# Kernel tuning notes

Hardware: AMD Instinct MI355X
Metric: run time of the kernel (lower is better)

The kernel has to match this reference:

```python
import jax, jax.numpy as jnp
import numpy as np

BATCH = 4096
LATENT = 2048
ZDIM = 128
TEMP = 0.5
PRIOR = 0.3
PRIOR_PRIME = 0.5
GAMMA = 1.0
BETA = 0.0
EPS = 1e-8  # torch CosineSimilarity eps


def setup_inputs() -> dict:
    key = jax.random.key(0)
    k = jax.random.split(key, 6)
    return {
        "h_i": jax.random.normal(k[0], (BATCH, LATENT), dtype=jnp.float32),
        "h_j": jax.random.normal(k[1], (BATCH, LATENT), dtype=jnp.float32),
        "z_i": jax.random.normal(k[2], (BATCH, ZDIM), dtype=jnp.float32),
        "z_j": jax.random.normal(k[3], (BATCH, ZDIM), dtype=jnp.float32),
        "target": jax.random.randint(k[4], (BATCH, 1), 0, 2, dtype=jnp.int64 if jax.config.jax_enable_x64 else jnp.int32),
        "W": jax.random.normal(k[5], (1, LATENT), dtype=jnp.float32) * (1.0 / np.sqrt(LATENT)),
        "b": jnp.zeros((1,), dtype=jnp.float32),
        "weight_onnpu": jnp.asarray(0.5, dtype=jnp.float32),
    }


def _onnpu_loss(inp, target):
    # inp: [B, 1] classifier logit; target: [B, 1] in {0, 1} -> {-1, +1}
    t = (target * 2 - 1).astype(inp.dtype)
    positive = (t == 1).astype(inp.dtype)
    unlabeled = (t == -1).astype(inp.dtype)
    one = jnp.asarray(1.0, inp.dtype)
    n_pos = jnp.maximum(one, jnp.sum(positive))
    n_unl = jnp.maximum(one, jnp.sum(unlabeled))
    sig = jax.nn.sigmoid  # loss(x) = sigmoid(-x)
    y_pos = sig(-(positive * inp)) * positive
    y_pos_inv = sig(positive * inp) * positive
    y_unl = sig(unlabeled * inp) * unlabeled
    positive_risk = PRIOR_PRIME / n_pos * jnp.sum(y_pos)
    negative_risk = ((1.0 - PRIOR_PRIME) / (n_unl * (1.0 - PRIOR)) * jnp.sum(y_unl)
                     - (1.0 - PRIOR_PRIME) * PRIOR / (n_pos * (1.0 - PRIOR)) * jnp.sum(y_pos_inv))
    # nnPU correction (nnPU=True, beta=0, gamma=1)
    return jnp.where(negative_risk < -BETA, -GAMMA * negative_risk,
                     positive_risk + negative_risk)


def _nt_xent_loss(z_i, z_j):
    B = z_i.shape[0]
    N = 2 * B
    z = jnp.concatenate([z_i, z_j], axis=0)  # [N, D]
    zn = z / jnp.maximum(jnp.linalg.norm(z, axis=1, keepdims=True), EPS)
    sim = (zn @ zn.T) / TEMP  # [N, N] cosine similarity / temperature
    idx = jnp.arange(N)
    pos = sim[idx, (idx + B) % N]  # positive pair logit per row
    # CE over [positive | all-other-than-self]: denominator is logsumexp over
    # the row with the self-similarity (diagonal) excluded.
    sim_masked = jnp.where(idx[:, None] == idx[None, :], -jnp.inf, sim)
    lse = jax.nn.logsumexp(sim_masked, axis=1)
    return jnp.sum(lse - pos) / N


def reference(h_i, h_j, z_i, z_j, target, W, b, weight_onnpu):
    logit_i = h_i @ W.T + b  # [B, 1]
    logit_j = h_j @ W.T + b
    onnpu_l = 0.5 * (_onnpu_loss(logit_i, target) + _onnpu_loss(logit_j, target))
    nt_xent_l = _nt_xent_loss(z_i, z_j)
    return weight_onnpu * onnpu_l + (1.0 - weight_onnpu) * nt_xent_l
```

## Files before the change

### kernel.cpp

```cpp
#include <hip/hip_runtime.h>

#define BATCH  4096
#define NROWS  8192
#define LATENT 2048
#define ZDIM   128
#define PRIORc       0.3f
#define PRIOR_PRIMEc 0.5f

#define NSIM 2080

typedef __attribute__((ext_vector_type(8))) short bf16x8;
typedef __attribute__((ext_vector_type(4))) float f32x4;

__device__ inline unsigned short f2bf_rne(float f) {
    unsigned int u = __float_as_uint(f);
    u = u + 0x7fffu + ((u >> 16) & 1u);
    return (unsigned short)(u >> 16);
}

__device__ inline float wave_reduce_sum(float v) {
#pragma unroll
    for (int m = 1; m < 64; m <<= 1) v += __shfl_xor(v, m, 64);
    return v;
}

__device__ inline void gload_lds16(const void* g, void* l) {
    __builtin_amdgcn_global_load_lds(
        (const __attribute__((address_space(1))) unsigned int*)g,
        (__attribute__((address_space(3))) unsigned int*)l, 16, 0, 0);
}

#define ZSCALE 1.69864464f

__global__ void k_zprep(const float* __restrict__ z_i, const float* __restrict__ z_j,
                        unsigned short* __restrict__ znb, float* __restrict__ pos,
                        float* __restrict__ dexp, float* __restrict__ S_row) {
    int bid = blockIdx.x;
    int wave = threadIdx.x >> 6, lane = threadIdx.x & 63;
    if (threadIdx.x < 8) S_row[bid * 8 + threadIdx.x] = 0.f;
    int r = bid * 4 + wave;
    int p = r + BATCH;
    float2 a = ((const float2*)(z_i + (size_t)r * ZDIM))[lane];
    float2 c = ((const float2*)(z_j + (size_t)r * ZDIM))[lane];
    float sa = wave_reduce_sum(a.x * a.x + a.y * a.y);
    float sc = wave_reduce_sum(c.x * c.x + c.y * c.y);
    float dd = wave_reduce_sum(a.x * c.x + a.y * c.y);
    float inva = 1.f / fmaxf(sqrtf(sa), 1e-8f);
    float invc = 1.f / fmaxf(sqrtf(sc), 1e-8f);
    if (lane == 0) {
        float pv = 2.0f * dd * inva * invc;
        pos[r] = pv;
        pos[p] = pv;
    }
    int kt = lane >> 4;
    int q  = (lane >> 2) & 3;
    int j  = (lane & 3) * 2;
    int lrow = q * 16;
    float fa = inva * ZSCALE, fc = invc * ZSCALE;
    ushort2 wa; wa.x = f2bf_rne(a.x * fa); wa.y = f2bf_rne(a.y * fa);
    ushort2 wc; wc.x = f2bf_rne(c.x * fc); wc.y = f2bf_rne(c.y * fc);
    {
        size_t off = ((size_t)((r >> 4) * 4 + kt) * 64 + (lrow + (r & 15))) * 8 + j;
        *(ushort2*)(znb + off) = wa;
    }
    {
        size_t off = ((size_t)((p >> 4) * 4 + kt) * 64 + (lrow + (p & 15))) * 8 + j;
        *(ushort2*)(znb + off) = wc;
    }
    float ax = __uint_as_float((unsigned)wa.x << 16);
    float ay = __uint_as_float((unsigned)wa.y << 16);
    float cx = __uint_as_float((unsigned)wc.x << 16);
    float cy = __uint_as_float((unsigned)wc.y << 16);
    float da = wave_reduce_sum(ax * ax + ay * ay);
    float dc = wave_reduce_sum(cx * cx + cy * cy);
    if (lane == 0) {
        dexp[r] = __builtin_amdgcn_exp2f(da);
        dexp[p] = __builtin_amdgcn_exp2f(dc);
    }
}

__global__ void __launch_bounds__(256, 4) k_main(
        const unsigned short* __restrict__ znb, float* __restrict__ S_row,
        const float* __restrict__ h_i, const float* __restrict__ h_j,
        const float* __restrict__ W, const float* __restrict__ bb,
        float* __restrict__ logits) {
    int bid = blockIdx.x;
    int lane = threadIdx.x & 63, wave = threadIdx.x >> 6;
    if (bid < NSIM) {
        int k = bid;
        int i = (int)((129.0f - sqrtf(16641.0f - 8.0f * (float)k)) * 0.5f);
        if (i > 63) i = 63;
        while (i * (129 - i) / 2 > k) --i;
        while ((i + 1) * (128 - i) / 2 <= k) ++i;
        int j = i + (k - i * (129 - i) / 2);
        bool diag = (i == j);

        int q = lane >> 4, t = lane & 15;
        int row0 = i * 128 + (wave >> 1) * 64;
        int gA = row0 >> 4;

        __shared__ __align__(16) unsigned char bpan[32768];
        __shared__ float red[256];

        {
            const unsigned char* gsrc = (const unsigned char*)znb + (size_t)j * 32768;
#pragma unroll
            for (int u = 0; u < 8; ++u) {
                int boff = u * 4096 + wave * 1024 + lane * 16;
                gload_lds16(gsrc + boff, bpan + u * 4096 + wave * 1024);
            }
        }
        red[threadIdx.x] = 0.f;

        const bf16x8* zf = (const bf16x8*)znb;
        bf16x8 a[4][4];
#pragma unroll
        for (int mt = 0; mt < 4; ++mt)
#pragma unroll
            for (int kt = 0; kt < 4; ++kt)
                a[mt][kt] = zf[(size_t)((gA + mt) * 4 + kt) * 64 + lane];

        float s[16];
#pragma unroll
        for (int idx = 0; idx < 16; ++idx) s[idx] = 0.f;
        float c[4];

        __syncthreads();

#pragma unroll
        for (int nt = 0; nt < 4; ++nt) {
            bf16x8 b[4];
#pragma unroll
            for (int kt = 0; kt < 4; ++kt)
                b[kt] = *(const bf16x8*)(bpan +
                        ((size_t)(((wave & 1) * 4 + nt) * 4 + kt) * 1024) + lane * 16);
            f32x4 acc[4];
            f32x4 zero = {0.f, 0.f, 0.f, 0.f};
#pragma unroll
            for (int mt = 0; mt < 4; ++mt) acc[mt] = zero;
#pragma unroll
            for (int kt = 0; kt < 4; ++kt)
#pragma unroll
                for (int mt = 0; mt < 4; ++mt)
                    acc[mt] = __builtin_amdgcn_mfma_f32_16x16x32_bf16(a[mt][kt], b[kt], acc[mt], 0, 0, 0);
            float csum = 0.f;
#pragma unroll
            for (int mt = 0; mt < 4; ++mt)
#pragma unroll
                for (int reg = 0; reg < 4; ++reg) {
                    float e = __builtin_amdgcn_exp2f(acc[mt][reg]);
                    s[mt * 4 + reg] += e;
                    csum += e;
                }
            c[nt] = csum;
        }

#pragma unroll
        for (int idx = 0; idx < 16; ++idx) {
            float v = s[idx];
            v += __shfl_xor(v, 1, 64);
            v += __shfl_xor(v, 2, 64);
            v += __shfl_xor(v, 4, 64);
            v += __shfl_xor(v, 8, 64);
            if (t == 0)
                atomicAdd(&red[(wave >> 1) * 64 + (idx >> 2) * 16 + q * 4 + (idx & 3)], v);
        }
#pragma unroll
        for (int nt = 0; nt < 4; ++nt) {
            float v = c[nt];
            v += __shfl_xor(v, 16, 64);
            v += __shfl_xor(v, 32, 64);
            if (q == 0)
                atomicAdd(&red[128 + (wave & 1) * 64 + nt * 16 + t], v);
        }
        __syncthreads();
        if (threadIdx.x < 128) {
            atomicAdd(&S_row[i * 128 + threadIdx.x], red[threadIdx.x]);
        } else if (!diag) {
            atomicAdd(&S_row[j * 128 + (threadIdx.x & 127)], red[threadIdx.x]);
        }
    } else {
        int r = (bid - NSIM) * 4 + wave;
        const float* h = (r < BATCH) ? (h_i + (size_t)r * LATENT)
                                     : (h_j + (size_t)(r - BATCH) * LATENT);
        const f32x4* h4 = (const f32x4*)h;
        const f32x4* w4 = (const f32x4*)W;
        float s = 0.f;
#pragma unroll
        for (int itr = 0; itr < 8; ++itr) {
            f32x4 av = h4[itr * 64 + lane];
            f32x4 wv = w4[itr * 64 + lane];
            s += av.x * wv.x + av.y * wv.y + av.z * wv.z + av.w * wv.w;
        }
        s = wave_reduce_sum(s);
        if (lane == 0) logits[r] = s + bb[0];
    }
}

__global__ void k_final(const float* __restrict__ S_row, const float* __restrict__ pos,
                        const float* __restrict__ dexp, const float* __restrict__ logits,
                        const int* __restrict__ target,
                        const float* __restrict__ w_onnpu, float* __restrict__ out) {
    float nt_s = 0.f;
    for (int r = threadIdx.x; r < NROWS; r += 1024)
        nt_s += __logf(S_row[r] - dexp[r]) - pos[r];
    float v[8];
#pragma unroll
    for (int i = 0; i < 8; ++i) v[i] = 0.f;
    for (int r = threadIdx.x; r < BATCH; r += 1024) {
        float li = logits[r], lj = logits[BATCH + r];
        bool p = (target[r] == 1);
        float si_n = 1.f / (1.f + __expf(li));
        float si_p = 1.f / (1.f + __expf(-li));
        float sj_n = 1.f / (1.f + __expf(lj));
        float sj_p = 1.f / (1.f + __expf(-lj));
        v[0] += p ? 1.f : 0.f;
        v[1] += p ? 0.f : 1.f;
        v[2] += p ? si_n : 0.f;
        v[3] += p ? si_p : 0.f;
        v[4] += p ? 0.f : si_p;
        v[5] += p ? sj_n : 0.f;
        v[6] += p ? sj_p : 0.f;
        v[7] += p ? 0.f : sj_p;
    }
    __shared__ float red[16][9];
    int wave = threadIdx.x >> 6, lane = threadIdx.x & 63;
    nt_s = wave_reduce_sum(nt_s);
#pragma unroll
    for (int i = 0; i < 8; ++i) v[i] = wave_reduce_sum(v[i]);
    if (lane == 0) {
        red[wave][0] = nt_s;
#pragma unroll
        for (int i = 0; i < 8; ++i) red[wave][1 + i] = v[i];
    }
    __syncthreads();
    if (threadIdx.x == 0) {
        float t[9];
#pragma unroll
        for (int i = 0; i < 9; ++i) {
            float acc = 0.f;
#pragma unroll
            for (int wv = 0; wv < 16; ++wv) acc += red[wv][i];
            t[i] = acc;
        }
        float ntxent = t[0] / (float)NROWS;
        float np = fmaxf(1.f, t[1]), nu = fmaxf(1.f, t[2]);
        float pr_i = PRIOR_PRIMEc / np * t[3];
        float nr_i = (1.f - PRIOR_PRIMEc) / (nu * (1.f - PRIORc)) * t[5]
                   - (1.f - PRIOR_PRIMEc) * PRIORc / (np * (1.f - PRIORc)) * t[4];
        float li_loss = (nr_i < 0.f) ? -nr_i : (pr_i + nr_i);
        float pr_j = PRIOR_PRIMEc / np * t[6];
        float nr_j = (1.f - PRIOR_PRIMEc) / (nu * (1.f - PRIORc)) * t[8]
                   - (1.f - PRIOR_PRIMEc) * PRIORc / (np * (1.f - PRIORc)) * t[7];
        float lj_loss = (nr_j < 0.f) ? -nr_j : (pr_j + nr_j);
        float onnpu = 0.5f * (li_loss + lj_loss);
        float w = w_onnpu[0];
        out[0] = w * onnpu + (1.f - w) * ntxent;
    }
}

extern "C" void kernel_launch(void* const* d_in, const int* in_sizes, int n_in,
                              void* d_out, int out_size, void* d_ws, size_t ws_size,
                              hipStream_t stream) {
    const float* h_i = (const float*)d_in[0];
    const float* h_j = (const float*)d_in[1];
    const float* z_i = (const float*)d_in[2];
    const float* z_j = (const float*)d_in[3];
    const int* target = (const int*)d_in[4];
    const float* W = (const float*)d_in[5];
    const float* b = (const float*)d_in[6];
    const float* w_onnpu = (const float*)d_in[7];

    char* ws = (char*)d_ws;
    unsigned short* znb = (unsigned short*)ws;
    float* S_row  = (float*)(ws + 2097152);
    float* pos    = (float*)(ws + 2097152 + 32768);
    float* logits = (float*)(ws + 2097152 + 65536);
    float* dexp   = (float*)(ws + 2097152 + 98304);
    float* out = (float*)d_out;

    k_zprep<<<1024, 256, 0, stream>>>(z_i, z_j, znb, pos, dexp, S_row);
    k_main<<<NSIM + 2048, 256, 0, stream>>>(znb, S_row, h_i, h_j, W, b, logits);
    k_final<<<1, 1024, 0, stream>>>(S_row, pos, dexp, logits, target, w_onnpu, out);
}
```

Baseline: 132.1 us.

## Make similarity blocks persistent over paired stripes with double-buffered LDS panels

The similarity part now runs as 512 persistent blocks instead of 2080 one-tile blocks. Each group of 16 blocks handles a complementary pair of row stripes (i and 63-i) to balance the triangular workload. Each block iterates over tiles while double-buffering the B panel in LDS via async global-to-LDS loads. Row sums stay in registers across tiles of the same stripe and are flushed with global atomics, replacing the per-block LDS reduction, while column sums go straight to global atomics. This amortizes launch and A-fragment loads and overlaps loads with compute, at the cost of doubled LDS (occupancy drops to 2 blocks per CU) and more global atomic traffic.

```diff
diff --git a/kernel.cpp b/kernel.cpp
--- a/kernel.cpp
+++ b/kernel.cpp
@@ -7,7 +7,8 @@
 #define PRIORc       0.3f
 #define PRIOR_PRIMEc 0.5f
 
-#define NSIM 2080
+#define NSIMB 512
+#define NGEMV 2048
 
 typedef __attribute__((ext_vector_type(8))) short bf16x8;
 typedef __attribute__((ext_vector_type(4))) float f32x4;
@@ -79,80 +80,129 @@
     }
 }
 
-__global__ void __launch_bounds__(256, 4) k_main(
+__global__ void __launch_bounds__(256, 2) k_main(
         const unsigned short* __restrict__ znb, float* __restrict__ S_row,
         const float* __restrict__ h_i, const float* __restrict__ h_j,
         const float* __restrict__ W, const float* __restrict__ bb,
         float* __restrict__ logits) {
     int bid = blockIdx.x;
     int lane = threadIdx.x & 63, wave = threadIdx.x >> 6;
-    if (bid < NSIM) {
-        int k = bid;
-        int i = (int)((129.0f - sqrtf(16641.0f - 8.0f * (float)k)) * 0.5f);
-        if (i > 63) i = 63;
-        while (i * (129 - i) / 2 > k) --i;
-        while ((i + 1) * (128 - i) / 2 <= k) ++i;
-        int j = i + (k - i * (129 - i) / 2);
-        bool diag = (i == j);
-
+    if (bid < NSIMB) {
+        int pairIdx = bid >> 4;
+        int sub = bid & 15;
+        int i0 = pairIdx, i1 = 63 - pairIdx;
+        int n0 = 64 - i0;
         int q = lane >> 4, t = lane & 15;
-        int row0 = i * 128 + (wave >> 1) * 64;
-        int gA = row0 >> 4;
-
-        __shared__ __align__(16) unsigned char bpan[32768];
-        __shared__ float red[256];
+        const bf16x8* zf = (const bf16x8*)znb;
+
+        __shared__ __align__(16) unsigned char bpan[2][32768];
 
         {
-            const unsigned char* gsrc = (const unsigned char*)znb + (size_t)j * 32768;
-#pragma unroll
-            for (int u = 0; u < 8; ++u) {
-                int boff = u * 4096 + wave * 1024 + lane * 16;
-                gload_lds16(gsrc + boff, bpan + u * 4096 + wave * 1024);
+            int j0 = i0 + sub;
+            const unsigned char* gsrc = (const unsigned char*)znb + (size_t)j0 * 32768;
+#pragma unroll
+            for (int u = 0; u < 8; ++u)
+                gload_lds16(gsrc + u * 4096 + wave * 1024 + lane * 16,
+                            bpan[0] + u * 4096 + wave * 1024);
+        }
+
+        int stripe = i0;
+        bf16x8 a[4][4];
+        {
+            int gA = i0 * 8 + (wave >> 1) * 4;
+#pragma unroll
+            for (int mt = 0; mt < 4; ++mt)
+#pragma unroll
+                for (int kt = 0; kt < 4; ++kt)
+                    a[mt][kt] = zf[(size_t)((gA + mt) * 4 + kt) * 64 + lane];
+        }
+
+        float s[16];
+#pragma unroll
+        for (int idx = 0; idx < 16; ++idx) s[idx] = 0.f;
+
+        __syncthreads();
+
+        int buf = 0;
+        for (int p = sub; p < 65; p += 16) {
+            int pi = (p < n0) ? i0 : i1;
+            int pj = (p < n0) ? (i0 + p) : (i1 + (p - n0));
+
+            int pn = p + 16;
+            if (pn < 65) {
+                int nj = (pn < n0) ? (i0 + pn) : (i1 + (pn - n0));
+                const unsigned char* gsrc = (const unsigned char*)znb + (size_t)nj * 32768;
+#pragma unroll
+                for (int u = 0; u < 8; ++u)
+                    gload_lds16(gsrc + u * 4096 + wave * 1024 + lane * 16,
+                                bpan[buf ^ 1] + u * 4096 + wave * 1024);
             }
-        }
-        red[threadIdx.x] = 0.f;
-
-        const bf16x8* zf = (const bf16x8*)znb;
-        bf16x8 a[4][4];
-#pragma unroll
-        for (int mt = 0; mt < 4; ++mt)
-#pragma unroll
-            for (int kt = 0; kt < 4; ++kt)
-                a[mt][kt] = zf[(size_t)((gA + mt) * 4 + kt) * 64 + lane];
-
-        float s[16];
-#pragma unroll
-        for (int idx = 0; idx < 16; ++idx) s[idx] = 0.f;
-        float c[4];
-
-        __syncthreads();
-
-#pragma unroll
-        for (int nt = 0; nt < 4; ++nt) {
-            bf16x8 b[4];
-#pragma unroll
-            for (int kt = 0; kt < 4; ++kt)
-                b[kt] = *(const bf16x8*)(bpan +
-                        ((size_t)(((wave & 1) * 4 + nt) * 4 + kt) * 1024) + lane * 16);
-            f32x4 acc[4];
-            f32x4 zero = {0.f, 0.f, 0.f, 0.f};
-#pragma unroll
-            for (int mt = 0; mt < 4; ++mt) acc[mt] = zero;
-#pragma unroll
-            for (int kt = 0; kt < 4; ++kt)
+
+            if (pi != stripe) {
+#pragma unroll
+                for (int idx = 0; idx < 16; ++idx) {
+                    float v = s[idx];
+                    v += __shfl_xor(v, 1, 64);
+                    v += __shfl_xor(v, 2, 64);
+                    v += __shfl_xor(v, 4, 64);
+                    v += __shfl_xor(v, 8, 64);
+                    if (t == 0)
+                        atomicAdd(&S_row[stripe * 128 + (wave >> 1) * 64 +
+                                         (idx >> 2) * 16 + q * 4 + (idx & 3)], v);
+                }
+                stripe = pi;
+                int gA = pi * 8 + (wave >> 1) * 4;
 #pragma unroll
                 for (int mt = 0; mt < 4; ++mt)
-                    acc[mt] = __builtin_amdgcn_mfma_f32_16x16x32_bf16(a[mt][kt], b[kt], acc[mt], 0, 0, 0);
-            float csum = 0.f;
-#pragma unroll
-            for (int mt = 0; mt < 4; ++mt)
-#pragma unroll
-                for (int reg = 0; reg < 4; ++reg) {
-                    float e = __builtin_amdgcn_exp2f(acc[mt][reg]);
-                    s[mt * 4 + reg] += e;
-                    csum += e;
+#pragma unroll
+                    for (int kt = 0; kt < 4; ++kt)
+                        a[mt][kt] = zf[(size_t)((gA + mt) * 4 + kt) * 64 + lane];
+#pragma unroll
+                for (int idx = 0; idx < 16; ++idx) s[idx] = 0.f;
+            }
+
+            float c[4];
+#pragma unroll
+            for (int nt = 0; nt < 4; ++nt) {
+                bf16x8 b[4];
+#pragma unroll
+                for (int kt = 0; kt < 4; ++kt)
+                    b[kt] = *(const bf16x8*)(bpan[buf] +
+                            ((size_t)(((wave & 1) * 4 + nt) * 4 + kt) * 1024) + lane * 16);
+                f32x4 acc[4];
+                f32x4 zero = {0.f, 0.f, 0.f, 0.f};
+#pragma unroll
+                for (int mt = 0; mt < 4; ++mt) acc[mt] = zero;
+#pragma unroll
+                for (int kt = 0; kt < 4; ++kt)
+#pragma unroll
+                    for (int mt = 0; mt < 4; ++mt)
+                        acc[mt] = __builtin_amdgcn_mfma_f32_16x16x32_bf16(a[mt][kt], b[kt], acc[mt], 0, 0, 0);
+                float csum = 0.f;
+#pragma unroll
+                for (int mt = 0; mt < 4; ++mt)
+#pragma unroll
+                    for (int reg = 0; reg < 4; ++reg) {
+                        float e = __builtin_amdgcn_exp2f(acc[mt][reg]);
+                        s[mt * 4 + reg] += e;
+                        csum += e;
+                    }
+                c[nt] = csum;
+            }
+
+            if (pi != pj) {
+#pragma unroll
+                for (int nt = 0; nt < 4; ++nt) {
+                    float v = c[nt];
+                    v += __shfl_xor(v, 16, 64);
+                    v += __shfl_xor(v, 32, 64);
+                    if (q == 0)
+                        atomicAdd(&S_row[pj * 128 + (wave & 1) * 64 + nt * 16 + t], v);
                 }
-            c[nt] = csum;
+            }
+
+            __syncthreads();
+            buf ^= 1;
         }
 
 #pragma unroll
@@ -163,24 +213,11 @@
             v += __shfl_xor(v, 4, 64);
             v += __shfl_xor(v, 8, 64);
             if (t == 0)
-                atomicAdd(&red[(wave >> 1) * 64 + (idx >> 2) * 16 + q * 4 + (idx & 3)], v);
-        }
-#pragma unroll
-        for (int nt = 0; nt < 4; ++nt) {
-            float v = c[nt];
-            v += __shfl_xor(v, 16, 64);
-            v += __shfl_xor(v, 32, 64);
-            if (q == 0)
-                atomicAdd(&red[128 + (wave & 1) * 64 + nt * 16 + t], v);
-        }
-        __syncthreads();
-        if (threadIdx.x < 128) {
-            atomicAdd(&S_row[i * 128 + threadIdx.x], red[threadIdx.x]);
-        } else if (!diag) {
-            atomicAdd(&S_row[j * 128 + (threadIdx.x & 127)], red[threadIdx.x]);
+                atomicAdd(&S_row[stripe * 128 + (wave >> 1) * 64 +
+                                 (idx >> 2) * 16 + q * 4 + (idx & 3)], v);
         }
     } else {
-        int r = (bid - NSIM) * 4 + wave;
+        int r = (bid - NSIMB) * 4 + wave;
         const float* h = (r < BATCH) ? (h_i + (size_t)r * LATENT)
                                      : (h_j + (size_t)(r - BATCH) * LATENT);
         const f32x4* h4 = (const f32x4*)h;
@@ -280,6 +317,6 @@
     float* out = (float*)d_out;
 
     k_zprep<<<1024, 256, 0, stream>>>(z_i, z_j, znb, pos, dexp, S_row);
-    k_main<<<NSIM + 2048, 256, 0, stream>>>(znb, S_row, h_i, h_j, W, b, logits);
+    k_main<<<NSIMB + NGEMV, 256, 0, stream>>>(znb, S_row, h_i, h_j, W, b, logits);
     k_final<<<1, 1024, 0, stream>>>(S_row, pos, dexp, logits, target, w_onnpu, out);
 }
```

Result: no change. 132.4 us (+0.2%).
